# Performance work log

Hardware: AMD Instinct MI355X
Metric: run time of the kernel (lower is better)

## Reference

```python
import jax, jax.numpy as jnp
import numpy as np

N_E = 8192
E_DIM = 64
EPS = 1e-12  # torch F.normalize eps


def l2_normalize(x):
    n = jnp.linalg.norm(x, axis=-1, keepdims=True)
    return x / jnp.maximum(n, EPS)


def setup_inputs() -> dict:
    key = jax.random.key(0)
    k1, k2 = jax.random.split(key)
    z = jax.random.normal(k1, (8, E_DIM, 64, 64), dtype=jnp.float32)  # [B, C, H, W]
    # init: uniform(-1/n_e, 1/n_e) then L2-normalized (l2_norm=True)
    emb = jax.random.uniform(k2, (N_E, E_DIM), dtype=jnp.float32,
                             minval=-1.0 / N_E, maxval=1.0 / N_E)
    emb = l2_normalize(emb)
    return {"z": z, "embedding": emb}


def reference(z, embedding):
    # b c h w -> b h w c
    zt = jnp.transpose(z, (0, 2, 3, 1))
    zn = l2_normalize(zt)                      # l2_norm=True path
    z_flat = zn.reshape(-1, zn.shape[-1])      # [B*H*W, e_dim]
    e = l2_normalize(embedding)                # [n_e, e_dim]

    # squared L2 distances: ||z||^2 + ||e||^2 - 2 z e^T
    d = (jnp.sum(z_flat ** 2, axis=1, keepdims=True)
         + jnp.sum(e ** 2, axis=1)
         - 2.0 * jnp.einsum('bd,nd->bn', z_flat, e))  # [B*H*W, n_e]

    min_encoding_indices = jnp.argmin(d, axis=1)       # [B*H*W]
    z_q = e[min_encoding_indices].reshape(zn.shape)    # gather codebook

    # straight-through estimator (eval mode: commit_loss is None)
    z_q = zn + jax.lax.stop_gradient(z_q - zn)
    z_q = jnp.transpose(z_q, (0, 3, 1, 2))             # b h w c -> b c h w
    return z_q, min_encoding_indices
```

## Files before the change

### kernel.cpp

```cpp
#include <hip/hip_runtime.h>


#define NPIX 32768
#define NE   8192
#define EDIM 64
#define HW   4096
#define NSTAGE 128
#define KSPLIT 8
#define CPS  (NE / KSPLIT)
#define NSTG (CPS / NSTAGE)
#define MARGIN1 6.0e-4f
#define MARGIN2 3.0e-5f
#define NSET 2
#define RSCL 2048.0f
#define RINV 4.8828125e-4f

typedef _Float16 f16x8 __attribute__((ext_vector_type(8)));
typedef float f32x4  __attribute__((ext_vector_type(4)));

__device__ __forceinline__ short f2h_bits(float x) {
    _Float16 h = (_Float16)x;
    short s; __builtin_memcpy(&s, &h, 2); return s;
}
__device__ __forceinline__ float h_hi_f(float x) {
    return (float)(_Float16)x;
}
__device__ __forceinline__ unsigned int order_u32(float f) {
    unsigned int s = __float_as_uint(f);
    return (s & 0x80000000u) ? ~s : (s | 0x80000000u);
}
__device__ __forceinline__ void gload_lds16(const void* g, void* l) {
    __builtin_amdgcn_global_load_lds(
        (const __attribute__((address_space(1))) void*)g,
        (__attribute__((address_space(3))) void*)l, 16, 0, 0);
}

__global__ __launch_bounds__(256) void k_prep(const float* __restrict__ emb,
                                              const float* __restrict__ z,
                                              float* __restrict__ e_norm,
                                              float* __restrict__ se_half,
                                              short* __restrict__ esw,
                                              short* __restrict__ eswl,
                                              float* __restrict__ zn,
                                              unsigned* __restrict__ counter) {
    if (blockIdx.x == 0 && threadIdx.x == 0) { counter[0] = 0u; counter[1] = 0u; }
    if (blockIdx.x < NE / 4) {
        const int wave = threadIdx.x >> 6;
        const int lane = threadIdx.x & 63;
        const int n = blockIdx.x * 4 + wave;
        float v = emb[n * EDIM + lane];
        float ss = v * v;
        #pragma unroll
        for (int off = 32; off; off >>= 1) ss += __shfl_xor(ss, off, 64);
        const float inv = 1.0f / fmaxf(sqrtf(ss), 1e-12f);
        const float en = v * inv;
        e_norm[n * EDIM + lane] = en;
        const float hf = h_hi_f(en);
        const int grp = n >> 6, cs = n & 63;
        const int sub = cs >> 4, colb = cs & 15;
        const int o = lane >> 3, j = lane & 7;
        const int slot = ((o & 3) * 16 + colb) * 8 + j;
        const int off16 = grp * 4096 + (sub * 2 + (o >> 2)) * 512 + slot;
        esw[off16]  = f2h_bits(en);
        eswl[off16] = f2h_bits((en - hf) * RSCL);
        float s2 = en * en;
        #pragma unroll
        for (int off = 32; off; off >>= 1) s2 += __shfl_xor(s2, off, 64);
        if (lane == 0) se_half[n] = 0.5f * s2;
    } else {
        const int p = (blockIdx.x - NE / 4) * 256 + threadIdx.x;
        const int b = p >> 12, hw = p & (HW - 1);
        const float* zp = z + b * (EDIM * HW) + hw;
        float v[EDIM];
        #pragma unroll
        for (int c = 0; c < EDIM; ++c) v[c] = zp[c * HW];
        float ss = 0.0f;
        #pragma unroll
        for (int c = 0; c < EDIM; ++c) ss = fmaf(v[c], v[c], ss);
        const float inv = 1.0f / fmaxf(sqrtf(ss), 1e-12f);
        #pragma unroll
        for (int c4 = 0; c4 < 16; ++c4) {
            float4 o;
            o.x = v[c4 * 4 + 0] * inv;
            o.y = v[c4 * 4 + 1] * inv;
            o.z = v[c4 * 4 + 2] * inv;
            o.w = v[c4 * 4 + 3] * inv;
            *(float4*)(zn + p * EDIM + c4 * 4) = o;
        }
    }
}

__global__ __launch_bounds__(256, 1) void k_mfma(const float* __restrict__ zn,
                                                 const short* __restrict__ esw,
                                                 float2* __restrict__ pv,
                                                 unsigned* __restrict__ pi)
{
    __shared__ __align__(16) short es[2][NSTAGE * EDIM];

    const int tid  = threadIdx.x;
    const int wave = tid >> 6, lane = tid & 63;
    const int quad = lane >> 4, col = lane & 15;
    const int p0   = blockIdx.x * 128 + wave * 32;
    const int g    = blockIdx.y;
    const int kbase = g * CPS;

    f16x8 ah[NSET][2];
    #pragma unroll
    for (int s = 0; s < NSET; ++s) {
        const float* zr = zn + (p0 + s * 16 + col) * EDIM;
        #pragma unroll
        for (int kc = 0; kc < 2; ++kc) {
            float f[8];
            *(float4*)(f + 0) = *(const float4*)(zr + kc * 32 + quad * 8 + 0);
            *(float4*)(f + 4) = *(const float4*)(zr + kc * 32 + quad * 8 + 4);
            #pragma unroll
            for (int i = 0; i < 8; ++i) ah[s][kc][i] = (_Float16)f[i];
        }
    }

    float b1[NSET][4], b2[NSET][4];
    #pragma unroll
    for (int s = 0; s < NSET; ++s)
        #pragma unroll
        for (int r = 0; r < 4; ++r) { b1[s][r] = 0.0f; b2[s][r] = 0.0f; }

    const f32x4 cini = {2.0f, 2.0f, 2.0f, 2.0f};

    const int combo0 = wave * 4;
    const char* gsrc0 = (const char*)esw + (size_t)kbase * 128
                        + combo0 * 1024 + lane * 16;
    #pragma unroll
    for (int it = 0; it < 4; ++it)
        gload_lds16(gsrc0 + it * 1024, (char*)&es[0][0] + (combo0 + it) * 1024);

    for (int nb = 0; nb < NSTG; ++nb) {
        const int cur = nb & 1;
        __syncthreads();
        if (nb + 1 < NSTG) {
            const char* gsrc = gsrc0 + (size_t)(nb + 1) * (NSTAGE * EDIM * 2);
            #pragma unroll
            for (int it = 0; it < 4; ++it)
                gload_lds16(gsrc + it * 1024,
                            (char*)&es[cur ^ 1][0] + (combo0 + it) * 1024);
        }

        const short* esb = es[cur];
        #pragma unroll
        for (int sub = 0; sub < 8; ++sub) {
            const short* base = esb + sub * 1024;
            const f16x8 bh0 = *(const f16x8*)(base + lane * 8);
            const f16x8 bh1 = *(const f16x8*)(base + 512 + lane * 8);
            const unsigned sid = (unsigned)((nb << 3) | sub);
            #pragma unroll
            for (int s = 0; s < NSET; ++s) {
                f32x4 acc;
                acc = __builtin_amdgcn_mfma_f32_16x16x32_f16(ah[s][0], bh0, cini, 0, 0, 0);
                acc = __builtin_amdgcn_mfma_f32_16x16x32_f16(ah[s][1], bh1, acc, 0, 0, 0);
                #pragma unroll
                for (int r = 0; r < 4; ++r) {
                    const float v = __uint_as_float(
                        (__float_as_uint(acc[r]) & 0xFFFFFFC0u) | sid);
                    b2[s][r] = __builtin_amdgcn_fmed3f(v, b2[s][r], b1[s][r]);
                    b1[s][r] = fmaxf(b1[s][r], v);
                }
            }
        }
    }

    int i1[NSET][4];
    #pragma unroll
    for (int s = 0; s < NSET; ++s)
        #pragma unroll
        for (int r = 0; r < 4; ++r) {
            const unsigned id6 = __float_as_uint(b1[s][r]) & 63u;
            i1[s][r] = kbase + (int)(id6 << 4) + col;
        }

    #pragma unroll
    for (int m = 1; m <= 8; m <<= 1) {
        #pragma unroll
        for (int s = 0; s < NSET; ++s)
            #pragma unroll
            for (int r = 0; r < 4; ++r) {
                const float ob1 = __shfl_xor(b1[s][r], m, 64);
                const int   oi1 = __shfl_xor(i1[s][r], m, 64);
                const float ob2 = __shfl_xor(b2[s][r], m, 64);
                const bool take = (ob1 > b1[s][r]) || (ob1 == b1[s][r] && oi1 < i1[s][r]);
                b2[s][r] = fmaxf(fmaxf(b2[s][r], ob2), fminf(b1[s][r], ob1));
                b1[s][r] = take ? ob1 : b1[s][r];
                i1[s][r] = take ? oi1 : i1[s][r];
            }
    }
    if (col == 0) {
        #pragma unroll
        for (int s = 0; s < NSET; ++s)
            #pragma unroll
            for (int r = 0; r < 4; ++r) {
                const int p = p0 + s * 16 + quad * 4 + r;
                pv[g * NPIX + p] = make_float2(b1[s][r], b2[s][r]);
                pi[g * NPIX + p] = (unsigned)i1[s][r];
            }
    }
}

__global__ __launch_bounds__(256) void k_merge(const float2* __restrict__ pv,
                                               const unsigned* __restrict__ pi,
                                               unsigned* __restrict__ idx_arr,
                                               unsigned* __restrict__ list,
                                               unsigned* __restrict__ counter,
                                               unsigned long long* __restrict__ packed) {
    const int p = blockIdx.x * 256 + threadIdx.x;
    float2 v[KSPLIT]; unsigned ix[KSPLIT];
    #pragma unroll
    for (int gg = 0; gg < KSPLIT; ++gg) { v[gg] = pv[gg * NPIX + p]; ix[gg] = pi[gg * NPIX + p]; }
    float b1 = v[0].x; unsigned i1 = ix[0]; int win = 0;
    #pragma unroll
    for (int gg = 1; gg < KSPLIT; ++gg)
        if (v[gg].x > b1) { b1 = v[gg].x; i1 = ix[gg]; win = gg; }
    float b2 = -3.0e38f;
    #pragma unroll
    for (int gg = 0; gg < KSPLIT; ++gg) {
        b2 = fmaxf(b2, v[gg].y);
        if (gg != win) b2 = fmaxf(b2, v[gg].x);
    }
    const bool fl = (b1 - b2 < MARGIN1);
    idx_arr[p] = i1 | (fl ? 0x80000000u : 0u);
    if (fl) {
        packed[p] = ~0ull;
        const unsigned pos = atomicAdd(&counter[0], 1u);
        if (pos < NPIX) list[pos] = p;
    }
}

__global__ __launch_bounds__(256, 1) void k_rechk2(const float* __restrict__ zn,
                                                   const short* __restrict__ esw,
                                                   const short* __restrict__ eswl,
                                                   const unsigned* __restrict__ list,
                                                   const unsigned* __restrict__ counter,
                                                   float2* __restrict__ pv,
                                                   unsigned* __restrict__ pi)
{
    __shared__ __align__(16) short es[2][2][NSTAGE * EDIM];

    int cnt = (int)counter[0]; if (cnt > NPIX) cnt = NPIX;
    const int ib = blockIdx.x * 128;
    if (ib >= cnt) return;

    const int tid  = threadIdx.x;
    const int wave = tid >> 6, lane = tid & 63;
    const int quad = lane >> 4, col = lane & 15;
    const int g    = blockIdx.y;
    const int kbase = g * CPS;

    f16x8 ah[NSET][2], al[NSET][2];
    #pragma unroll
    for (int s = 0; s < NSET; ++s) {
        int item = ib + wave * 32 + s * 16 + col;
        if (item > cnt - 1) item = cnt - 1;
        const float* zr = zn + (size_t)list[item] * EDIM;
        #pragma unroll
        for (int kc = 0; kc < 2; ++kc) {
            float f[8];
            *(float4*)(f + 0) = *(const float4*)(zr + kc * 32 + quad * 8 + 0);
            *(float4*)(f + 4) = *(const float4*)(zr + kc * 32 + quad * 8 + 4);
            #pragma unroll
            for (int i = 0; i < 8; ++i) {
                ah[s][kc][i] = (_Float16)f[i];
                al[s][kc][i] = (_Float16)((f[i] - h_hi_f(f[i])) * RSCL);
            }
        }
    }

    float b1[NSET][4], b2[NSET][4]; int i1[NSET][4];
    #pragma unroll
    for (int s = 0; s < NSET; ++s)
        #pragma unroll
        for (int r = 0; r < 4; ++r) { b1[s][r] = 0.0f; b2[s][r] = 0.0f; i1[s][r] = 0; }

    const f32x4 cini = {2.0f, 2.0f, 2.0f, 2.0f};
    const f32x4 zero = {0.0f, 0.0f, 0.0f, 0.0f};

    const int combo0 = wave * 4;
    const char* ghi0 = (const char*)esw  + (size_t)kbase * 128 + combo0 * 1024 + lane * 16;
    const char* glo0 = (const char*)eswl + (size_t)kbase * 128 + combo0 * 1024 + lane * 16;
    #pragma unroll
    for (int it = 0; it < 4; ++it) {
        gload_lds16(ghi0 + it * 1024, (char*)&es[0][0][0] + (combo0 + it) * 1024);
        gload_lds16(glo0 + it * 1024, (char*)&es[0][1][0] + (combo0 + it) * 1024);
    }

    for (int nb = 0; nb < NSTG; ++nb) {
        const int cur = nb & 1;
        const int n0 = kbase + nb * NSTAGE;
        __syncthreads();
        if (nb + 1 < NSTG) {
            const size_t soff = (size_t)(nb + 1) * (NSTAGE * EDIM * 2);
            #pragma unroll
            for (int it = 0; it < 4; ++it) {
                gload_lds16(ghi0 + soff + it * 1024,
                            (char*)&es[cur ^ 1][0][0] + (combo0 + it) * 1024);
                gload_lds16(glo0 + soff + it * 1024,
                            (char*)&es[cur ^ 1][1][0] + (combo0 + it) * 1024);
            }
        }

        const short* eh = es[cur][0];
        const short* el = es[cur][1];
        #pragma unroll
        for (int sub = 0; sub < 8; ++sub) {
            const f16x8 bh0 = *(const f16x8*)(eh + sub * 1024 + lane * 8);
            const f16x8 bh1 = *(const f16x8*)(eh + sub * 1024 + 512 + lane * 8);
            const f16x8 bl0 = *(const f16x8*)(el + sub * 1024 + lane * 8);
            const f16x8 bl1 = *(const f16x8*)(el + sub * 1024 + 512 + lane * 8);
            const int nglob = n0 + sub * 16 + col;
            #pragma unroll
            for (int s = 0; s < NSET; ++s) {
                f32x4 acc;
                acc = __builtin_amdgcn_mfma_f32_16x16x32_f16(ah[s][0], bh0, cini, 0, 0, 0);
                acc = __builtin_amdgcn_mfma_f32_16x16x32_f16(ah[s][1], bh1, acc, 0, 0, 0);
                f32x4 cor;
                cor = __builtin_amdgcn_mfma_f32_16x16x32_f16(al[s][0], bh0, zero, 0, 0, 0);
                cor = __builtin_amdgcn_mfma_f32_16x16x32_f16(ah[s][0], bl0, cor, 0, 0, 0);
                cor = __builtin_amdgcn_mfma_f32_16x16x32_f16(al[s][1], bh1, cor, 0, 0, 0);
                cor = __builtin_amdgcn_mfma_f32_16x16x32_f16(ah[s][1], bl1, cor, 0, 0, 0);
                #pragma unroll
                for (int r = 0; r < 4; ++r) {
                    const float v = fmaf(cor[r], RINV, acc[r]);
                    b2[s][r] = __builtin_amdgcn_fmed3f(v, b2[s][r], b1[s][r]);
                    const bool t = v > b1[s][r];
                    b1[s][r] = fmaxf(b1[s][r], v);
                    i1[s][r] = t ? nglob : i1[s][r];
                }
            }
        }
    }

    #pragma unroll
    for (int m = 1; m <= 8; m <<= 1) {
        #pragma unroll
        for (int s = 0; s < NSET; ++s)
            #pragma unroll
            for (int r = 0; r < 4; ++r) {
                const float ob1 = __shfl_xor(b1[s][r], m, 64);
                const int   oi1 = __shfl_xor(i1[s][r], m, 64);
                const float ob2 = __shfl_xor(b2[s][r], m, 64);
                const bool take = (ob1 > b1[s][r]) || (ob1 == b1[s][r] && oi1 < i1[s][r]);
                b2[s][r] = fmaxf(fmaxf(b2[s][r], ob2), fminf(b1[s][r], ob1));
                b1[s][r] = take ? ob1 : b1[s][r];
                i1[s][r] = take ? oi1 : i1[s][r];
            }
    }
    if (col == 0) {
        #pragma unroll
        for (int s = 0; s < NSET; ++s)
            #pragma unroll
            for (int r = 0; r < 4; ++r) {
                const int item = ib + wave * 32 + s * 16 + quad * 4 + r;
                if (item < cnt) {
                    pv[g * NPIX + item] = make_float2(b1[s][r], b2[s][r]);
                    pi[g * NPIX + item] = (unsigned)i1[s][r];
                }
            }
    }
}

__global__ __launch_bounds__(256) void k_merge2(const float2* __restrict__ pv,
                                                const unsigned* __restrict__ pi,
                                                const unsigned* __restrict__ list,
                                                unsigned* __restrict__ counter,
                                                unsigned* __restrict__ list2,
                                                unsigned long long* __restrict__ packed) {
    const int item = blockIdx.x * 256 + threadIdx.x;
    int cnt = (int)counter[0]; if (cnt > NPIX) cnt = NPIX;
    if (item >= cnt) return;
    const unsigned p = list[item];
    float2 v[KSPLIT]; unsigned ix[KSPLIT];
    #pragma unroll
    for (int gg = 0; gg < KSPLIT; ++gg) { v[gg] = pv[gg * NPIX + item]; ix[gg] = pi[gg * NPIX + item]; }
    float b1 = v[0].x; unsigned i1 = ix[0]; int win = 0;
    #pragma unroll
    for (int gg = 1; gg < KSPLIT; ++gg)
        if (v[gg].x > b1) { b1 = v[gg].x; i1 = ix[gg]; win = gg; }
    float b2 = -3.0e38f;
    #pragma unroll
    for (int gg = 0; gg < KSPLIT; ++gg) {
        b2 = fmaxf(b2, v[gg].y);
        if (gg != win) b2 = fmaxf(b2, v[gg].x);
    }
    if (b1 - b2 < MARGIN2) {
        const unsigned pos = atomicAdd(&counter[1], 1u);
        if (pos < NPIX) list2[pos] = p;
    } else {
        packed[p] = (unsigned long long)i1;
    }
}

__global__ __launch_bounds__(256) void k_recheck(const float* __restrict__ zn,
                                                 const float* __restrict__ e_norm,
                                                 const float* __restrict__ se_half,
                                                 const unsigned* __restrict__ list2,
                                                 const unsigned* __restrict__ counter,
                                                 unsigned long long* __restrict__ packed) {
    const int lane  = threadIdx.x & 63;
    const int k     = lane >> 4;
    const int m     = lane & 15;
    const int wglob = (blockIdx.x * 256 + threadIdx.x) >> 6;
    const int nwav  = (gridDim.x * 256) >> 6;
    int cnt = (int)counter[1]; if (cnt > NPIX) cnt = NPIX;
    const int nitems = cnt * 16;
    const float4* e4 = (const float4*)e_norm;

    for (int item = wglob; item < nitems; item += nwav) {
        const int p     = (int)list2[item >> 4];
        const int chunk = item & 15;
        const float4 zv = *(const float4*)(zn + p * EDIM + m * 4);
        float best = 3.0e38f; int bidx = 0;
        for (int t4 = 0; t4 < 32; ++t4) {
            float s[4]; int n[4];
            #pragma unroll
            for (int j = 0; j < 4; ++j) {
                n[j] = chunk * 512 + (t4 * 4 + j) * 4 + k;
                const float4 ev = e4[n[j] * 16 + m];
                s[j] = fmaf(zv.w, ev.w, fmaf(zv.z, ev.z,
                       fmaf(zv.y, ev.y, zv.x * ev.x)));
            }
            #pragma unroll
            for (int j = 0; j < 4; ++j) s[j] += __shfl_xor(s[j], 1, 64);
            #pragma unroll
            for (int j = 0; j < 4; ++j) s[j] += __shfl_xor(s[j], 2, 64);
            #pragma unroll
            for (int j = 0; j < 4; ++j) s[j] += __shfl_xor(s[j], 4, 64);
            #pragma unroll
            for (int j = 0; j < 4; ++j) s[j] += __shfl_xor(s[j], 8, 64);
            #pragma unroll
            for (int j = 0; j < 4; ++j) {
                const float d = se_half[n[j]] - s[j];
                if (d < best) { best = d; bidx = n[j]; }
            }
        }
        #pragma unroll
        for (int mm = 1; mm <= 32; mm <<= 1) {
            const float ob = __shfl_xor(best, mm, 64);
            const int   oi = __shfl_xor(bidx, mm, 64);
            if (ob < best || (ob == best && oi < bidx)) { best = ob; bidx = oi; }
        }
        if (lane == 0) {
            const unsigned long long key =
                ((unsigned long long)order_u32(best) << 32) | (unsigned)bidx;
            atomicMin(&packed[p], key);
        }
    }
}

__global__ __launch_bounds__(256) void k_finalize(const unsigned* __restrict__ idx_arr,
                                                  const unsigned long long* __restrict__ packed,
                                                  const float* __restrict__ e_norm,
                                                  float* __restrict__ out) {
    const int pl = threadIdx.x & 63;
    const int q  = threadIdx.x >> 6;
    const int p  = blockIdx.x * 64 + pl;
    const unsigned v = idx_arr[p];
    const int bidx = (v & 0x80000000u) ? (int)(packed[p] & 0xFFFFFFFFull)
                                       : (int)v;
    if (q == 0) out[NPIX * EDIM + p] = (float)bidx;
    const int b = p >> 12, hw = p & (HW - 1);
    float* op = out + b * (EDIM * HW) + hw;
    const float4* ep4 = (const float4*)(e_norm + bidx * EDIM + q * 16);
    #pragma unroll
    for (int j = 0; j < 4; ++j) {
        const float4 e = ep4[j];
        const int c = q * 16 + j * 4;
        op[(c + 0) * HW] = e.x; op[(c + 1) * HW] = e.y;
        op[(c + 2) * HW] = e.z; op[(c + 3) * HW] = e.w;
    }
}

extern "C" void kernel_launch(void* const* d_in, const int* in_sizes, int n_in,
                              void* d_out, int out_size, void* d_ws, size_t ws_size,
                              hipStream_t stream) {
    const float* z   = (const float*)d_in[0];
    const float* emb = (const float*)d_in[1];
    float* out = (float*)d_out;

    float* e_norm  = (float*)d_ws;
    float* se_half = e_norm + NE * EDIM;
    short* esw  = (short*)(se_half + NE);
    short* eswl = esw + NE * EDIM;
    float* zn = (float*)(eswl + NE * EDIM);
    unsigned* idx_arr = (unsigned*)(zn + NPIX * EDIM);
    unsigned* list    = idx_arr + NPIX;
    unsigned* list2   = list + NPIX;
    unsigned* counter = list2 + NPIX;
    unsigned long long* packed = (unsigned long long*)(counter + 64);
    float2*   pv = (float2*)(packed + NPIX);
    unsigned* pi = (unsigned*)(pv + KSPLIT * NPIX);

    k_prep<<<NE / 4 + NPIX / 256, 256, 0, stream>>>(emb, z, e_norm, se_half,
                                                    esw, eswl, zn, counter);
    k_mfma<<<dim3(NPIX / 128, KSPLIT), 256, 0, stream>>>(zn, esw, pv, pi);
    k_merge<<<NPIX / 256, 256, 0, stream>>>(pv, pi, idx_arr, list, counter, packed);
    k_rechk2<<<dim3(NPIX / 128, KSPLIT), 256, 0, stream>>>(zn, esw, eswl, list,
                                                           counter, pv, pi);
    k_merge2<<<NPIX / 256, 256, 0, stream>>>(pv, pi, list, counter, list2, packed);
    k_recheck<<<512, 256, 0, stream>>>(zn, e_norm, se_half, list2, counter, packed);
    k_finalize<<<NPIX / 64, 256, 0, stream>>>(idx_arr, packed, e_norm, out);
}
```

Measured before the change: 188.3 us.

## Fuse second merge, exact recheck and finalize; split refine pass 32 ways

Removes the k_merge2, k_recheck and k_finalize kernels and the packed atomicMin buffer. A single k_final kernel now merges the refinement partials, runs the exact fp32 rescan per block for escaped pixels, and writes the outputs. The refine kernel now uses a capped list of 8192 items and splits the codebook 32 ways instead of 8, giving more blocks for a small candidate list. This cuts two launches and their global round trips. In exchange, escaped pixels are rescanned serially inside a block, and pixels beyond the 8192 cap fall back to a full exact scan.

```diff
diff --git a/kernel.cpp b/kernel.cpp
--- a/kernel.cpp
+++ b/kernel.cpp
@@ -9,6 +9,10 @@
 #define KSPLIT 8
 #define CPS  (NE / KSPLIT)
 #define NSTG (CPS / NSTAGE)
+#define KS2  32
+#define CPS2 (NE / KS2)
+#define NSTG2 (CPS2 / NSTAGE)
+#define CAP2 8192
 #define MARGIN1 6.0e-4f
 #define MARGIN2 3.0e-5f
 #define NSET 2
@@ -43,7 +47,7 @@
                                               short* __restrict__ eswl,
                                               float* __restrict__ zn,
                                               unsigned* __restrict__ counter) {
-    if (blockIdx.x == 0 && threadIdx.x == 0) { counter[0] = 0u; counter[1] = 0u; }
+    if (blockIdx.x == 0 && threadIdx.x == 0) { counter[0] = 0u; }
     if (blockIdx.x < NE / 4) {
         const int wave = threadIdx.x >> 6;
         const int lane = threadIdx.x & 63;
@@ -207,8 +211,7 @@
                                                const unsigned* __restrict__ pi,
                                                unsigned* __restrict__ idx_arr,
                                                unsigned* __restrict__ list,
-                                               unsigned* __restrict__ counter,
-                                               unsigned long long* __restrict__ packed) {
+                                               unsigned* __restrict__ counter) {
     const int p = blockIdx.x * 256 + threadIdx.x;
     float2 v[KSPLIT]; unsigned ix[KSPLIT];
     #pragma unroll
@@ -223,12 +226,12 @@
         b2 = fmaxf(b2, v[gg].y);
         if (gg != win) b2 = fmaxf(b2, v[gg].x);
     }
-    const bool fl = (b1 - b2 < MARGIN1);
-    idx_arr[p] = i1 | (fl ? 0x80000000u : 0u);
-    if (fl) {
-        packed[p] = ~0ull;
+    if (b1 - b2 < MARGIN1) {
         const unsigned pos = atomicAdd(&counter[0], 1u);
-        if (pos < NPIX) list[pos] = p;
+        if (pos < CAP2) list[pos] = p;
+        idx_arr[p] = 0x80000000u | pos;
+    } else {
+        idx_arr[p] = i1;
     }
 }
 
@@ -242,15 +245,15 @@
 {
     __shared__ __align__(16) short es[2][2][NSTAGE * EDIM];
 
-    int cnt = (int)counter[0]; if (cnt > NPIX) cnt = NPIX;
+    int cnt = (int)counter[0]; if (cnt > CAP2) cnt = CAP2;
     const int ib = blockIdx.x * 128;
     if (ib >= cnt) return;
 
     const int tid  = threadIdx.x;
     const int wave = tid >> 6, lane = tid & 63;
     const int quad = lane >> 4, col = lane & 15;
-    const int g    = blockIdx.y;
-    const int kbase = g * CPS;
+    const int g2   = blockIdx.y;
+    const int kbase = g2 * CPS2;
 
     f16x8 ah[NSET][2], al[NSET][2];
     #pragma unroll
@@ -289,11 +292,11 @@
         gload_lds16(glo0 + it * 1024, (char*)&es[0][1][0] + (combo0 + it) * 1024);
     }
 
-    for (int nb = 0; nb < NSTG; ++nb) {
+    for (int nb = 0; nb < NSTG2; ++nb) {
         const int cur = nb & 1;
         const int n0 = kbase + nb * NSTAGE;
         __syncthreads();
-        if (nb + 1 < NSTG) {
+        if (nb + 1 < NSTG2) {
             const size_t soff = (size_t)(nb + 1) * (NSTAGE * EDIM * 2);
             #pragma unroll
             for (int it = 0; it < 4; ++it) {
@@ -357,85 +360,92 @@
             for (int r = 0; r < 4; ++r) {
                 const int item = ib + wave * 32 + s * 16 + quad * 4 + r;
                 if (item < cnt) {
-                    pv[g * NPIX + item] = make_float2(b1[s][r], b2[s][r]);
-                    pi[g * NPIX + item] = (unsigned)i1[s][r];
+                    pv[g2 * CAP2 + item] = make_float2(b1[s][r], b2[s][r]);
+                    pi[g2 * CAP2 + item] = (unsigned)i1[s][r];
                 }
             }
     }
 }
 
-__global__ __launch_bounds__(256) void k_merge2(const float2* __restrict__ pv,
-                                                const unsigned* __restrict__ pi,
-                                                const unsigned* __restrict__ list,
-                                                unsigned* __restrict__ counter,
-                                                unsigned* __restrict__ list2,
-                                                unsigned long long* __restrict__ packed) {
-    const int item = blockIdx.x * 256 + threadIdx.x;
-    int cnt = (int)counter[0]; if (cnt > NPIX) cnt = NPIX;
-    if (item >= cnt) return;
-    const unsigned p = list[item];
-    float2 v[KSPLIT]; unsigned ix[KSPLIT];
-    #pragma unroll
-    for (int gg = 0; gg < KSPLIT; ++gg) { v[gg] = pv[gg * NPIX + item]; ix[gg] = pi[gg * NPIX + item]; }
-    float b1 = v[0].x; unsigned i1 = ix[0]; int win = 0;
-    #pragma unroll
-    for (int gg = 1; gg < KSPLIT; ++gg)
-        if (v[gg].x > b1) { b1 = v[gg].x; i1 = ix[gg]; win = gg; }
-    float b2 = -3.0e38f;
-    #pragma unroll
-    for (int gg = 0; gg < KSPLIT; ++gg) {
-        b2 = fmaxf(b2, v[gg].y);
-        if (gg != win) b2 = fmaxf(b2, v[gg].x);
-    }
-    if (b1 - b2 < MARGIN2) {
-        const unsigned pos = atomicAdd(&counter[1], 1u);
-        if (pos < NPIX) list2[pos] = p;
-    } else {
-        packed[p] = (unsigned long long)i1;
-    }
-}
-
-__global__ __launch_bounds__(256) void k_recheck(const float* __restrict__ zn,
-                                                 const float* __restrict__ e_norm,
-                                                 const float* __restrict__ se_half,
-                                                 const unsigned* __restrict__ list2,
-                                                 const unsigned* __restrict__ counter,
-                                                 unsigned long long* __restrict__ packed) {
-    const int lane  = threadIdx.x & 63;
-    const int k     = lane >> 4;
-    const int m     = lane & 15;
-    const int wglob = (blockIdx.x * 256 + threadIdx.x) >> 6;
-    const int nwav  = (gridDim.x * 256) >> 6;
-    int cnt = (int)counter[1]; if (cnt > NPIX) cnt = NPIX;
-    const int nitems = cnt * 16;
-    const float4* e4 = (const float4*)e_norm;
-
-    for (int item = wglob; item < nitems; item += nwav) {
-        const int p     = (int)list2[item >> 4];
-        const int chunk = item & 15;
-        const float4 zv = *(const float4*)(zn + p * EDIM + m * 4);
+__global__ __launch_bounds__(256) void k_final(const unsigned* __restrict__ idx_arr,
+                                               const float2* __restrict__ pv,
+                                               const unsigned* __restrict__ pi,
+                                               const float* __restrict__ e_norm,
+                                               const float* __restrict__ zn,
+                                               const float* __restrict__ se_half,
+                                               float* __restrict__ out) {
+    __shared__ int s_bidx[64];
+    __shared__ int s_escp[64];
+    __shared__ int s_esc;
+    __shared__ unsigned long long s_key[4];
+
+    const int tid  = threadIdx.x;
+    const int wave = tid >> 6, lane = tid & 63;
+    const int p0   = blockIdx.x * 64;
+
+    if (tid == 0) s_esc = 0;
+    __syncthreads();
+
+    if (wave == 0) {
+        const unsigned v = idx_arr[p0 + lane];
+        int bidx;
+        if (!(v & 0x80000000u)) {
+            bidx = (int)v;
+        } else {
+            const unsigned item = v & 0x7FFFFFFFu;
+            if (item >= CAP2) {
+                bidx = -1;
+            } else {
+                float b1 = -3.0e38f, b2 = -3.0e38f; unsigned i1 = 0;
+                #pragma unroll
+                for (int g2 = 0; g2 < KS2; ++g2) {
+                    const float2 vv = pv[g2 * CAP2 + item];
+                    const unsigned ii = pi[g2 * CAP2 + item];
+                    if (vv.x > b1) { b2 = fmaxf(b2, b1); b1 = vv.x; i1 = ii; }
+                    else           { b2 = fmaxf(b2, vv.x); }
+                    b2 = fmaxf(b2, vv.y);
+                }
+                bidx = (b1 - b2 < MARGIN2) ? -1 : (int)i1;
+            }
+        }
+        s_bidx[lane] = bidx;
+        if (bidx < 0) {
+            const int e = atomicAdd(&s_esc, 1);
+            s_escp[e] = lane;
+        }
+    }
+    __syncthreads();
+
+    const int nesc = s_esc;
+    for (int e = 0; e < nesc; ++e) {
+        const int p = p0 + s_escp[e];
+        const int k = lane >> 4, m = lane & 15;
+        const float4 zv = *(const float4*)(zn + (size_t)p * EDIM + m * 4);
+        const float4* e4 = (const float4*)e_norm;
         float best = 3.0e38f; int bidx = 0;
-        for (int t4 = 0; t4 < 32; ++t4) {
-            float s[4]; int n[4];
-            #pragma unroll
-            for (int j = 0; j < 4; ++j) {
-                n[j] = chunk * 512 + (t4 * 4 + j) * 4 + k;
-                const float4 ev = e4[n[j] * 16 + m];
-                s[j] = fmaf(zv.w, ev.w, fmaf(zv.z, ev.z,
-                       fmaf(zv.y, ev.y, zv.x * ev.x)));
-            }
-            #pragma unroll
-            for (int j = 0; j < 4; ++j) s[j] += __shfl_xor(s[j], 1, 64);
-            #pragma unroll
-            for (int j = 0; j < 4; ++j) s[j] += __shfl_xor(s[j], 2, 64);
-            #pragma unroll
-            for (int j = 0; j < 4; ++j) s[j] += __shfl_xor(s[j], 4, 64);
-            #pragma unroll
-            for (int j = 0; j < 4; ++j) s[j] += __shfl_xor(s[j], 8, 64);
-            #pragma unroll
-            for (int j = 0; j < 4; ++j) {
-                const float d = se_half[n[j]] - s[j];
-                if (d < best) { best = d; bidx = n[j]; }
+        for (int chunk = wave; chunk < 16; chunk += 4) {
+            for (int t4 = 0; t4 < 32; ++t4) {
+                float sdot[4]; int n[4];
+                #pragma unroll
+                for (int j = 0; j < 4; ++j) {
+                    n[j] = chunk * 512 + (t4 * 4 + j) * 4 + k;
+                    const float4 ev = e4[n[j] * 16 + m];
+                    sdot[j] = fmaf(zv.w, ev.w, fmaf(zv.z, ev.z,
+                              fmaf(zv.y, ev.y, zv.x * ev.x)));
+                }
+                #pragma unroll
+                for (int j = 0; j < 4; ++j) sdot[j] += __shfl_xor(sdot[j], 1, 64);
+                #pragma unroll
+                for (int j = 0; j < 4; ++j) sdot[j] += __shfl_xor(sdot[j], 2, 64);
+                #pragma unroll
+                for (int j = 0; j < 4; ++j) sdot[j] += __shfl_xor(sdot[j], 4, 64);
+                #pragma unroll
+                for (int j = 0; j < 4; ++j) sdot[j] += __shfl_xor(sdot[j], 8, 64);
+                #pragma unroll
+                for (int j = 0; j < 4; ++j) {
+                    const float d = se_half[n[j]] - sdot[j];
+                    if (d < best) { best = d; bidx = n[j]; }
+                }
             }
         }
         #pragma unroll
@@ -444,34 +454,31 @@
             const int   oi = __shfl_xor(bidx, mm, 64);
             if (ob < best || (ob == best && oi < bidx)) { best = ob; bidx = oi; }
         }
-        if (lane == 0) {
-            const unsigned long long key =
-                ((unsigned long long)order_u32(best) << 32) | (unsigned)bidx;
-            atomicMin(&packed[p], key);
-        }
-    }
-}
-
-__global__ __launch_bounds__(256) void k_finalize(const unsigned* __restrict__ idx_arr,
-                                                  const unsigned long long* __restrict__ packed,
-                                                  const float* __restrict__ e_norm,
-                                                  float* __restrict__ out) {
-    const int pl = threadIdx.x & 63;
-    const int q  = threadIdx.x >> 6;
-    const int p  = blockIdx.x * 64 + pl;
-    const unsigned v = idx_arr[p];
-    const int bidx = (v & 0x80000000u) ? (int)(packed[p] & 0xFFFFFFFFull)
-                                       : (int)v;
+        if (lane == 0)
+            s_key[wave] = ((unsigned long long)order_u32(best) << 32) | (unsigned)bidx;
+        __syncthreads();
+        if (tid == 0) {
+            unsigned long long kk = s_key[0];
+            #pragma unroll
+            for (int w = 1; w < 4; ++w) kk = (s_key[w] < kk) ? s_key[w] : kk;
+            s_bidx[s_escp[e]] = (int)(kk & 0xFFFFFFFFull);
+        }
+        __syncthreads();
+    }
+
+    const int p = p0 + lane;
+    const int bidx = s_bidx[lane];
+    const int q = wave;
     if (q == 0) out[NPIX * EDIM + p] = (float)bidx;
     const int b = p >> 12, hw = p & (HW - 1);
     float* op = out + b * (EDIM * HW) + hw;
-    const float4* ep4 = (const float4*)(e_norm + bidx * EDIM + q * 16);
+    const float4* ep4 = (const float4*)(e_norm + (size_t)bidx * EDIM + q * 16);
     #pragma unroll
     for (int j = 0; j < 4; ++j) {
-        const float4 e = ep4[j];
+        const float4 ev = ep4[j];
         const int c = q * 16 + j * 4;
-        op[(c + 0) * HW] = e.x; op[(c + 1) * HW] = e.y;
-        op[(c + 2) * HW] = e.z; op[(c + 3) * HW] = e.w;
+        op[(c + 0) * HW] = ev.x; op[(c + 1) * HW] = ev.y;
+        op[(c + 2) * HW] = ev.z; op[(c + 3) * HW] = ev.w;
     }
 }
 
@@ -489,19 +496,16 @@
     float* zn = (float*)(eswl + NE * EDIM);
     unsigned* idx_arr = (unsigned*)(zn + NPIX * EDIM);
     unsigned* list    = idx_arr + NPIX;
-    unsigned* list2   = list + NPIX;
-    unsigned* counter = list2 + NPIX;
-    unsigned long long* packed = (unsigned long long*)(counter + 64);
-    float2*   pv = (float2*)(packed + NPIX);
+    unsigned* counter = list + NPIX;
+    float2*   pv = (float2*)(counter + 64);
     unsigned* pi = (unsigned*)(pv + KSPLIT * NPIX);
 
     k_prep<<<NE / 4 + NPIX / 256, 256, 0, stream>>>(emb, z, e_norm, se_half,
                                                     esw, eswl, zn, counter);
     k_mfma<<<dim3(NPIX / 128, KSPLIT), 256, 0, stream>>>(zn, esw, pv, pi);
-    k_merge<<<NPIX / 256, 256, 0, stream>>>(pv, pi, idx_arr, list, counter, packed);
-    k_rechk2<<<dim3(NPIX / 128, KSPLIT), 256, 0, stream>>>(zn, esw, eswl, list,
-                                                           counter, pv, pi);
-    k_merge2<<<NPIX / 256, 256, 0, stream>>>(pv, pi, list, counter, list2, packed);
-    k_recheck<<<512, 256, 0, stream>>>(zn, e_norm, se_half, list2, counter, packed);
-    k_finalize<<<NPIX / 64, 256, 0, stream>>>(idx_arr, packed, e_norm, out);
-}
+    k_merge<<<NPIX / 256, 256, 0, stream>>>(pv, pi, idx_arr, list, counter);
+    k_rechk2<<<dim3(CAP2 / 128, KS2), 256, 0, stream>>>(zn, esw, eswl, list,
+                                                        counter, pv, pi);
+    k_final<<<NPIX / 64, 256, 0, stream>>>(idx_arr, pv, pi, e_norm, zn,
+                                           se_half, out);
+}
```

Result: slower. 299.5 us (+59.0%).

## Restructure MFMA argmin with per-wave codebook slices and capped finer-split recheck

Applied to the files above, without the earlier changes.

The main MFMA pass now gives each wave its own slice of the codebook chunk, with private LDS double buffers and explicit vmcnt waits instead of block-wide barriers. Each block handles 64 pixels, so every wave carries 4 A-fragment sets, and the per-wave top-2 results are merged through shared memory. The refinement pass is capped at 8192 flagged pixels with a 32-way codebook split to spread the small work list over more blocks. Flagged pixels beyond the cap go straight to the exact fp32 recheck, whose grid is doubled. This trades more register pressure and an extra LDS merge for fewer synchronisations and better parallelism in the recheck stage.

```diff
diff --git a/kernel.cpp b/kernel.cpp
--- a/kernel.cpp
+++ b/kernel.cpp
@@ -5,13 +5,15 @@
 #define NE   8192
 #define EDIM 64
 #define HW   4096
-#define NSTAGE 128
 #define KSPLIT 8
 #define CPS  (NE / KSPLIT)
-#define NSTG (CPS / NSTAGE)
+#define NSTAGE 128
+#define KS2  32
+#define CPS2 (NE / KS2)
+#define NSTG2 (CPS2 / NSTAGE)
+#define CAP2 8192
 #define MARGIN1 6.0e-4f
 #define MARGIN2 3.0e-5f
-#define NSET 2
 #define RSCL 2048.0f
 #define RINV 4.8828125e-4f
 
@@ -95,18 +97,21 @@
                                                  float2* __restrict__ pv,
                                                  unsigned* __restrict__ pi)
 {
-    __shared__ __align__(16) short es[2][NSTAGE * EDIM];
+    __shared__ __align__(16) short es[4][2][2048];
+    __shared__ float s_b1[4][64], s_b2[4][64];
+    __shared__ int   s_i1[4][64];
 
     const int tid  = threadIdx.x;
-    const int wave = tid >> 6, lane = tid & 63;
+    const int w    = tid >> 6, lane = tid & 63;
     const int quad = lane >> 4, col = lane & 15;
-    const int p0   = blockIdx.x * 128 + wave * 32;
+    const int p0   = blockIdx.x * 64;
     const int g    = blockIdx.y;
     const int kbase = g * CPS;
-
-    f16x8 ah[NSET][2];
-    #pragma unroll
-    for (int s = 0; s < NSET; ++s) {
+    const int cbase = kbase + w * 256;
+
+    f16x8 ah[4][2];
+    #pragma unroll
+    for (int s = 0; s < 4; ++s) {
         const float* zr = zn + (p0 + s * 16 + col) * EDIM;
         #pragma unroll
         for (int kc = 0; kc < 2; ++kc) {
@@ -118,41 +123,41 @@
         }
     }
 
-    float b1[NSET][4], b2[NSET][4];
-    #pragma unroll
-    for (int s = 0; s < NSET; ++s)
+    float b1[4][4], b2[4][4];
+    #pragma unroll
+    for (int s = 0; s < 4; ++s)
         #pragma unroll
         for (int r = 0; r < 4; ++r) { b1[s][r] = 0.0f; b2[s][r] = 0.0f; }
 
     const f32x4 cini = {2.0f, 2.0f, 2.0f, 2.0f};
 
-    const int combo0 = wave * 4;
-    const char* gsrc0 = (const char*)esw + (size_t)kbase * 128
-                        + combo0 * 1024 + lane * 16;
+    const char* gw = (const char*)esw + (size_t)cbase * 128 + lane * 16;
     #pragma unroll
     for (int it = 0; it < 4; ++it)
-        gload_lds16(gsrc0 + it * 1024, (char*)&es[0][0] + (combo0 + it) * 1024);
-
-    for (int nb = 0; nb < NSTG; ++nb) {
+        gload_lds16(gw + it * 1024, (char*)&es[w][0][0] + it * 1024);
+
+    for (int nb = 0; nb < 8; ++nb) {
         const int cur = nb & 1;
-        __syncthreads();
-        if (nb + 1 < NSTG) {
-            const char* gsrc = gsrc0 + (size_t)(nb + 1) * (NSTAGE * EDIM * 2);
+        if (nb + 1 < 8) {
+            const char* gs = gw + (size_t)(nb + 1) * 4096;
             #pragma unroll
             for (int it = 0; it < 4; ++it)
-                gload_lds16(gsrc + it * 1024,
-                            (char*)&es[cur ^ 1][0] + (combo0 + it) * 1024);
-        }
-
-        const short* esb = es[cur];
-        #pragma unroll
-        for (int sub = 0; sub < 8; ++sub) {
+                gload_lds16(gs + it * 1024, (char*)&es[w][cur ^ 1][0] + it * 1024);
+            asm volatile("s_waitcnt vmcnt(4)" ::: "memory");
+        } else {
+            asm volatile("s_waitcnt vmcnt(0)" ::: "memory");
+        }
+        __builtin_amdgcn_sched_barrier(0);
+
+        const short* esb = &es[w][cur][0];
+        #pragma unroll
+        for (int sub = 0; sub < 2; ++sub) {
             const short* base = esb + sub * 1024;
             const f16x8 bh0 = *(const f16x8*)(base + lane * 8);
             const f16x8 bh1 = *(const f16x8*)(base + 512 + lane * 8);
-            const unsigned sid = (unsigned)((nb << 3) | sub);
-            #pragma unroll
-            for (int s = 0; s < NSET; ++s) {
+            const unsigned sid = (unsigned)((w << 4) | (nb << 1) | sub);
+            #pragma unroll
+            for (int s = 0; s < 4; ++s) {
                 f32x4 acc;
                 acc = __builtin_amdgcn_mfma_f32_16x16x32_f16(ah[s][0], bh0, cini, 0, 0, 0);
                 acc = __builtin_amdgcn_mfma_f32_16x16x32_f16(ah[s][1], bh1, acc, 0, 0, 0);
@@ -167,9 +172,9 @@
         }
     }
 
-    int i1[NSET][4];
-    #pragma unroll
-    for (int s = 0; s < NSET; ++s)
+    int i1[4][4];
+    #pragma unroll
+    for (int s = 0; s < 4; ++s)
         #pragma unroll
         for (int r = 0; r < 4; ++r) {
             const unsigned id6 = __float_as_uint(b1[s][r]) & 63u;
@@ -179,7 +184,7 @@
     #pragma unroll
     for (int m = 1; m <= 8; m <<= 1) {
         #pragma unroll
-        for (int s = 0; s < NSET; ++s)
+        for (int s = 0; s < 4; ++s)
             #pragma unroll
             for (int r = 0; r < 4; ++r) {
                 const float ob1 = __shfl_xor(b1[s][r], m, 64);
@@ -193,13 +198,30 @@
     }
     if (col == 0) {
         #pragma unroll
-        for (int s = 0; s < NSET; ++s)
+        for (int s = 0; s < 4; ++s)
             #pragma unroll
             for (int r = 0; r < 4; ++r) {
-                const int p = p0 + s * 16 + quad * 4 + r;
-                pv[g * NPIX + p] = make_float2(b1[s][r], b2[s][r]);
-                pi[g * NPIX + p] = (unsigned)i1[s][r];
-            }
+                const int px = s * 16 + quad * 4 + r;
+                s_b1[w][px] = b1[s][r];
+                s_b2[w][px] = b2[s][r];
+                s_i1[w][px] = i1[s][r];
+            }
+    }
+    __syncthreads();
+    if (w == 0) {
+        float B1 = s_b1[0][lane], B2 = s_b2[0][lane];
+        int   I1 = s_i1[0][lane];
+        #pragma unroll
+        for (int ww = 1; ww < 4; ++ww) {
+            const float ob1 = s_b1[ww][lane], ob2 = s_b2[ww][lane];
+            const int   oi1 = s_i1[ww][lane];
+            const bool take = ob1 > B1;
+            B2 = fmaxf(fmaxf(B2, ob2), fminf(B1, ob1));
+            B1 = take ? ob1 : B1;
+            I1 = take ? oi1 : I1;
+        }
+        pv[g * NPIX + p0 + lane] = make_float2(B1, B2);
+        pi[g * NPIX + p0 + lane] = (unsigned)I1;
     }
 }
 
@@ -207,6 +229,7 @@
                                                const unsigned* __restrict__ pi,
                                                unsigned* __restrict__ idx_arr,
                                                unsigned* __restrict__ list,
+                                               unsigned* __restrict__ list2,
                                                unsigned* __restrict__ counter,
                                                unsigned long long* __restrict__ packed) {
     const int p = blockIdx.x * 256 + threadIdx.x;
@@ -223,12 +246,18 @@
         b2 = fmaxf(b2, v[gg].y);
         if (gg != win) b2 = fmaxf(b2, v[gg].x);
     }
-    const bool fl = (b1 - b2 < MARGIN1);
-    idx_arr[p] = i1 | (fl ? 0x80000000u : 0u);
-    if (fl) {
+    if (b1 - b2 < MARGIN1) {
         packed[p] = ~0ull;
+        idx_arr[p] = i1 | 0x80000000u;
         const unsigned pos = atomicAdd(&counter[0], 1u);
-        if (pos < NPIX) list[pos] = p;
+        if (pos < CAP2) {
+            list[pos] = p;
+        } else {
+            const unsigned q = atomicAdd(&counter[1], 1u);
+            if (q < NPIX) list2[q] = p;
+        }
+    } else {
+        idx_arr[p] = i1;
     }
 }
 
@@ -242,19 +271,19 @@
 {
     __shared__ __align__(16) short es[2][2][NSTAGE * EDIM];
 
-    int cnt = (int)counter[0]; if (cnt > NPIX) cnt = NPIX;
+    int cnt = (int)counter[0]; if (cnt > CAP2) cnt = CAP2;
     const int ib = blockIdx.x * 128;
     if (ib >= cnt) return;
 
     const int tid  = threadIdx.x;
     const int wave = tid >> 6, lane = tid & 63;
     const int quad = lane >> 4, col = lane & 15;
-    const int g    = blockIdx.y;
-    const int kbase = g * CPS;
-
-    f16x8 ah[NSET][2], al[NSET][2];
-    #pragma unroll
-    for (int s = 0; s < NSET; ++s) {
+    const int g2   = blockIdx.y;
+    const int kbase = g2 * CPS2;
+
+    f16x8 ah[2][2], al[2][2];
+    #pragma unroll
+    for (int s = 0; s < 2; ++s) {
         int item = ib + wave * 32 + s * 16 + col;
         if (item > cnt - 1) item = cnt - 1;
         const float* zr = zn + (size_t)list[item] * EDIM;
@@ -271,9 +300,9 @@
         }
     }
 
-    float b1[NSET][4], b2[NSET][4]; int i1[NSET][4];
-    #pragma unroll
-    for (int s = 0; s < NSET; ++s)
+    float b1[2][4], b2[2][4]; int i1[2][4];
+    #pragma unroll
+    for (int s = 0; s < 2; ++s)
         #pragma unroll
         for (int r = 0; r < 4; ++r) { b1[s][r] = 0.0f; b2[s][r] = 0.0f; i1[s][r] = 0; }
 
@@ -289,11 +318,11 @@
         gload_lds16(glo0 + it * 1024, (char*)&es[0][1][0] + (combo0 + it) * 1024);
     }
 
-    for (int nb = 0; nb < NSTG; ++nb) {
+    for (int nb = 0; nb < NSTG2; ++nb) {
         const int cur = nb & 1;
         const int n0 = kbase + nb * NSTAGE;
         __syncthreads();
-        if (nb + 1 < NSTG) {
+        if (nb + 1 < NSTG2) {
             const size_t soff = (size_t)(nb + 1) * (NSTAGE * EDIM * 2);
             #pragma unroll
             for (int it = 0; it < 4; ++it) {
@@ -314,7 +343,7 @@
             const f16x8 bl1 = *(const f16x8*)(el + sub * 1024 + 512 + lane * 8);
             const int nglob = n0 + sub * 16 + col;
             #pragma unroll
-            for (int s = 0; s < NSET; ++s) {
+            for (int s = 0; s < 2; ++s) {
                 f32x4 acc;
                 acc = __builtin_amdgcn_mfma_f32_16x16x32_f16(ah[s][0], bh0, cini, 0, 0, 0);
                 acc = __builtin_amdgcn_mfma_f32_16x16x32_f16(ah[s][1], bh1, acc, 0, 0, 0);
@@ -338,7 +367,7 @@
     #pragma unroll
     for (int m = 1; m <= 8; m <<= 1) {
         #pragma unroll
-        for (int s = 0; s < NSET; ++s)
+        for (int s = 0; s < 2; ++s)
             #pragma unroll
             for (int r = 0; r < 4; ++r) {
                 const float ob1 = __shfl_xor(b1[s][r], m, 64);
@@ -352,13 +381,13 @@
     }
     if (col == 0) {
         #pragma unroll
-        for (int s = 0; s < NSET; ++s)
+        for (int s = 0; s < 2; ++s)
             #pragma unroll
             for (int r = 0; r < 4; ++r) {
                 const int item = ib + wave * 32 + s * 16 + quad * 4 + r;
                 if (item < cnt) {
-                    pv[g * NPIX + item] = make_float2(b1[s][r], b2[s][r]);
-                    pi[g * NPIX + item] = (unsigned)i1[s][r];
+                    pv[g2 * CAP2 + item] = make_float2(b1[s][r], b2[s][r]);
+                    pi[g2 * CAP2 + item] = (unsigned)i1[s][r];
                 }
             }
     }
@@ -371,25 +400,21 @@
                                                 unsigned* __restrict__ list2,
                                                 unsigned long long* __restrict__ packed) {
     const int item = blockIdx.x * 256 + threadIdx.x;
-    int cnt = (int)counter[0]; if (cnt > NPIX) cnt = NPIX;
+    int cnt = (int)counter[0]; if (cnt > CAP2) cnt = CAP2;
     if (item >= cnt) return;
     const unsigned p = list[item];
-    float2 v[KSPLIT]; unsigned ix[KSPLIT];
-    #pragma unroll
-    for (int gg = 0; gg < KSPLIT; ++gg) { v[gg] = pv[gg * NPIX + item]; ix[gg] = pi[gg * NPIX + item]; }
-    float b1 = v[0].x; unsigned i1 = ix[0]; int win = 0;
-    #pragma unroll
-    for (int gg = 1; gg < KSPLIT; ++gg)
-        if (v[gg].x > b1) { b1 = v[gg].x; i1 = ix[gg]; win = gg; }
-    float b2 = -3.0e38f;
-    #pragma unroll
-    for (int gg = 0; gg < KSPLIT; ++gg) {
-        b2 = fmaxf(b2, v[gg].y);
-        if (gg != win) b2 = fmaxf(b2, v[gg].x);
+    float b1 = -3.0e38f, b2 = -3.0e38f; unsigned i1 = 0;
+    #pragma unroll
+    for (int g2 = 0; g2 < KS2; ++g2) {
+        const float2 vv = pv[g2 * CAP2 + item];
+        const unsigned ii = pi[g2 * CAP2 + item];
+        if (vv.x > b1) { b2 = fmaxf(b2, b1); b1 = vv.x; i1 = ii; }
+        else           { b2 = fmaxf(b2, vv.x); }
+        b2 = fmaxf(b2, vv.y);
     }
     if (b1 - b2 < MARGIN2) {
-        const unsigned pos = atomicAdd(&counter[1], 1u);
-        if (pos < NPIX) list2[pos] = p;
+        const unsigned q = atomicAdd(&counter[1], 1u);
+        if (q < NPIX) list2[q] = p;
     } else {
         packed[p] = (unsigned long long)i1;
     }
@@ -413,7 +438,7 @@
     for (int item = wglob; item < nitems; item += nwav) {
         const int p     = (int)list2[item >> 4];
         const int chunk = item & 15;
-        const float4 zv = *(const float4*)(zn + p * EDIM + m * 4);
+        const float4 zv = *(const float4*)(zn + (size_t)p * EDIM + m * 4);
         float best = 3.0e38f; int bidx = 0;
         for (int t4 = 0; t4 < 32; ++t4) {
             float s[4]; int n[4];
@@ -465,7 +490,7 @@
     if (q == 0) out[NPIX * EDIM + p] = (float)bidx;
     const int b = p >> 12, hw = p & (HW - 1);
     float* op = out + b * (EDIM * HW) + hw;
-    const float4* ep4 = (const float4*)(e_norm + bidx * EDIM + q * 16);
+    const float4* ep4 = (const float4*)(e_norm + (size_t)bidx * EDIM + q * 16);
     #pragma unroll
     for (int j = 0; j < 4; ++j) {
         const float4 e = ep4[j];
@@ -497,11 +522,12 @@
 
     k_prep<<<NE / 4 + NPIX / 256, 256, 0, stream>>>(emb, z, e_norm, se_half,
                                                     esw, eswl, zn, counter);
-    k_mfma<<<dim3(NPIX / 128, KSPLIT), 256, 0, stream>>>(zn, esw, pv, pi);
-    k_merge<<<NPIX / 256, 256, 0, stream>>>(pv, pi, idx_arr, list, counter, packed);
-    k_rechk2<<<dim3(NPIX / 128, KSPLIT), 256, 0, stream>>>(zn, esw, eswl, list,
-                                                           counter, pv, pi);
-    k_merge2<<<NPIX / 256, 256, 0, stream>>>(pv, pi, list, counter, list2, packed);
-    k_recheck<<<512, 256, 0, stream>>>(zn, e_norm, se_half, list2, counter, packed);
+    k_mfma<<<dim3(NPIX / 64, KSPLIT), 256, 0, stream>>>(zn, esw, pv, pi);
+    k_merge<<<NPIX / 256, 256, 0, stream>>>(pv, pi, idx_arr, list, list2,
+                                            counter, packed);
+    k_rechk2<<<dim3(CAP2 / 128, KS2), 256, 0, stream>>>(zn, esw, eswl, list,
+                                                        counter, pv, pi);
+    k_merge2<<<CAP2 / 256, 256, 0, stream>>>(pv, pi, list, counter, list2, packed);
+    k_recheck<<<1024, 256, 0, stream>>>(zn, e_norm, se_half, list2, counter, packed);
     k_finalize<<<NPIX / 64, 256, 0, stream>>>(idx_arr, packed, e_norm, out);
 }
```

Result: slower. 248.9 us (+32.2%).

## Cap second-pass recheck list, split codebook 16 ways, overflow to exact pass

Applied to the files above, without the earlier changes.

The second-pass fp16 hi/lo MFMA recheck now splits the codebook into 16 chunks with smaller 64-code LDS stages, instead of 8 chunks with 128-code stages. This doubles parallelism for the flagged pixel list. The recheck list is capped at 16384 entries: overflow pixels go straight to the exact fp32 recheck list, and the grid sizes are reduced to match the cap. The merge step reduces 16 partials with a streaming top-2 update. The final fp32 recheck gets more blocks, and some index math is widened to size_t. The aim is to cut wasted blocks and raise occupancy for the recheck, at the cost of more partial-result traffic and a slower exact path for any overflow.

```diff
diff --git a/kernel.cpp b/kernel.cpp
--- a/kernel.cpp
+++ b/kernel.cpp
@@ -9,6 +9,11 @@
 #define KSPLIT 8
 #define CPS  (NE / KSPLIT)
 #define NSTG (CPS / NSTAGE)
+#define KS2  16
+#define CPS2 (NE / KS2)
+#define NST2 64
+#define NSTG2 (CPS2 / NST2)
+#define CAP2 16384
 #define MARGIN1 6.0e-4f
 #define MARGIN2 3.0e-5f
 #define NSET 2
@@ -207,6 +212,7 @@
                                                const unsigned* __restrict__ pi,
                                                unsigned* __restrict__ idx_arr,
                                                unsigned* __restrict__ list,
+                                               unsigned* __restrict__ list2,
                                                unsigned* __restrict__ counter,
                                                unsigned long long* __restrict__ packed) {
     const int p = blockIdx.x * 256 + threadIdx.x;
@@ -223,12 +229,18 @@
         b2 = fmaxf(b2, v[gg].y);
         if (gg != win) b2 = fmaxf(b2, v[gg].x);
     }
-    const bool fl = (b1 - b2 < MARGIN1);
-    idx_arr[p] = i1 | (fl ? 0x80000000u : 0u);
-    if (fl) {
+    if (b1 - b2 < MARGIN1) {
         packed[p] = ~0ull;
+        idx_arr[p] = i1 | 0x80000000u;
         const unsigned pos = atomicAdd(&counter[0], 1u);
-        if (pos < NPIX) list[pos] = p;
+        if (pos < CAP2) {
+            list[pos] = p;
+        } else {
+            const unsigned q = atomicAdd(&counter[1], 1u);
+            if (q < NPIX) list2[q] = p;
+        }
+    } else {
+        idx_arr[p] = i1;
     }
 }
 
@@ -240,17 +252,17 @@
                                                    float2* __restrict__ pv,
                                                    unsigned* __restrict__ pi)
 {
-    __shared__ __align__(16) short es[2][2][NSTAGE * EDIM];
-
-    int cnt = (int)counter[0]; if (cnt > NPIX) cnt = NPIX;
+    __shared__ __align__(16) short es[2][2][NST2 * EDIM];
+
+    int cnt = (int)counter[0]; if (cnt > CAP2) cnt = CAP2;
     const int ib = blockIdx.x * 128;
     if (ib >= cnt) return;
 
     const int tid  = threadIdx.x;
     const int wave = tid >> 6, lane = tid & 63;
     const int quad = lane >> 4, col = lane & 15;
-    const int g    = blockIdx.y;
-    const int kbase = g * CPS;
+    const int g2   = blockIdx.y;
+    const int kbase = g2 * CPS2;
 
     f16x8 ah[NSET][2], al[NSET][2];
     #pragma unroll
@@ -280,23 +292,23 @@
     const f32x4 cini = {2.0f, 2.0f, 2.0f, 2.0f};
     const f32x4 zero = {0.0f, 0.0f, 0.0f, 0.0f};
 
-    const int combo0 = wave * 4;
+    const int combo0 = wave * 2;
     const char* ghi0 = (const char*)esw  + (size_t)kbase * 128 + combo0 * 1024 + lane * 16;
     const char* glo0 = (const char*)eswl + (size_t)kbase * 128 + combo0 * 1024 + lane * 16;
     #pragma unroll
-    for (int it = 0; it < 4; ++it) {
+    for (int it = 0; it < 2; ++it) {
         gload_lds16(ghi0 + it * 1024, (char*)&es[0][0][0] + (combo0 + it) * 1024);
         gload_lds16(glo0 + it * 1024, (char*)&es[0][1][0] + (combo0 + it) * 1024);
     }
 
-    for (int nb = 0; nb < NSTG; ++nb) {
+    for (int nb = 0; nb < NSTG2; ++nb) {
         const int cur = nb & 1;
-        const int n0 = kbase + nb * NSTAGE;
+        const int n0 = kbase + nb * NST2;
         __syncthreads();
-        if (nb + 1 < NSTG) {
-            const size_t soff = (size_t)(nb + 1) * (NSTAGE * EDIM * 2);
-            #pragma unroll
-            for (int it = 0; it < 4; ++it) {
+        if (nb + 1 < NSTG2) {
+            const size_t soff = (size_t)(nb + 1) * (NST2 * EDIM * 2);
+            #pragma unroll
+            for (int it = 0; it < 2; ++it) {
                 gload_lds16(ghi0 + soff + it * 1024,
                             (char*)&es[cur ^ 1][0][0] + (combo0 + it) * 1024);
                 gload_lds16(glo0 + soff + it * 1024,
@@ -307,7 +319,7 @@
         const short* eh = es[cur][0];
         const short* el = es[cur][1];
         #pragma unroll
-        for (int sub = 0; sub < 8; ++sub) {
+        for (int sub = 0; sub < 4; ++sub) {
             const f16x8 bh0 = *(const f16x8*)(eh + sub * 1024 + lane * 8);
             const f16x8 bh1 = *(const f16x8*)(eh + sub * 1024 + 512 + lane * 8);
             const f16x8 bl0 = *(const f16x8*)(el + sub * 1024 + lane * 8);
@@ -357,8 +369,8 @@
             for (int r = 0; r < 4; ++r) {
                 const int item = ib + wave * 32 + s * 16 + quad * 4 + r;
                 if (item < cnt) {
-                    pv[g * NPIX + item] = make_float2(b1[s][r], b2[s][r]);
-                    pi[g * NPIX + item] = (unsigned)i1[s][r];
+                    pv[g2 * CAP2 + item] = make_float2(b1[s][r], b2[s][r]);
+                    pi[g2 * CAP2 + item] = (unsigned)i1[s][r];
                 }
             }
     }
@@ -371,25 +383,21 @@
                                                 unsigned* __restrict__ list2,
                                                 unsigned long long* __restrict__ packed) {
     const int item = blockIdx.x * 256 + threadIdx.x;
-    int cnt = (int)counter[0]; if (cnt > NPIX) cnt = NPIX;
+    int cnt = (int)counter[0]; if (cnt > CAP2) cnt = CAP2;
     if (item >= cnt) return;
     const unsigned p = list[item];
-    float2 v[KSPLIT]; unsigned ix[KSPLIT];
-    #pragma unroll
-    for (int gg = 0; gg < KSPLIT; ++gg) { v[gg] = pv[gg * NPIX + item]; ix[gg] = pi[gg * NPIX + item]; }
-    float b1 = v[0].x; unsigned i1 = ix[0]; int win = 0;
-    #pragma unroll
-    for (int gg = 1; gg < KSPLIT; ++gg)
-        if (v[gg].x > b1) { b1 = v[gg].x; i1 = ix[gg]; win = gg; }
-    float b2 = -3.0e38f;
-    #pragma unroll
-    for (int gg = 0; gg < KSPLIT; ++gg) {
-        b2 = fmaxf(b2, v[gg].y);
-        if (gg != win) b2 = fmaxf(b2, v[gg].x);
+    float b1 = -3.0e38f, b2 = -3.0e38f; unsigned i1 = 0;
+    #pragma unroll
+    for (int g2 = 0; g2 < KS2; ++g2) {
+        const float2 vv = pv[g2 * CAP2 + item];
+        const unsigned ii = pi[g2 * CAP2 + item];
+        if (vv.x > b1) { b2 = fmaxf(b2, b1); b1 = vv.x; i1 = ii; }
+        else           { b2 = fmaxf(b2, vv.x); }
+        b2 = fmaxf(b2, vv.y);
     }
     if (b1 - b2 < MARGIN2) {
-        const unsigned pos = atomicAdd(&counter[1], 1u);
-        if (pos < NPIX) list2[pos] = p;
+        const unsigned q = atomicAdd(&counter[1], 1u);
+        if (q < NPIX) list2[q] = p;
     } else {
         packed[p] = (unsigned long long)i1;
     }
@@ -413,7 +421,7 @@
     for (int item = wglob; item < nitems; item += nwav) {
         const int p     = (int)list2[item >> 4];
         const int chunk = item & 15;
-        const float4 zv = *(const float4*)(zn + p * EDIM + m * 4);
+        const float4 zv = *(const float4*)(zn + (size_t)p * EDIM + m * 4);
         float best = 3.0e38f; int bidx = 0;
         for (int t4 = 0; t4 < 32; ++t4) {
             float s[4]; int n[4];
@@ -465,7 +473,7 @@
     if (q == 0) out[NPIX * EDIM + p] = (float)bidx;
     const int b = p >> 12, hw = p & (HW - 1);
     float* op = out + b * (EDIM * HW) + hw;
-    const float4* ep4 = (const float4*)(e_norm + bidx * EDIM + q * 16);
+    const float4* ep4 = (const float4*)(e_norm + (size_t)bidx * EDIM + q * 16);
     #pragma unroll
     for (int j = 0; j < 4; ++j) {
         const float4 e = ep4[j];
@@ -498,10 +506,11 @@
     k_prep<<<NE / 4 + NPIX / 256, 256, 0, stream>>>(emb, z, e_norm, se_half,
                                                     esw, eswl, zn, counter);
     k_mfma<<<dim3(NPIX / 128, KSPLIT), 256, 0, stream>>>(zn, esw, pv, pi);
-    k_merge<<<NPIX / 256, 256, 0, stream>>>(pv, pi, idx_arr, list, counter, packed);
-    k_rechk2<<<dim3(NPIX / 128, KSPLIT), 256, 0, stream>>>(zn, esw, eswl, list,
-                                                           counter, pv, pi);
-    k_merge2<<<NPIX / 256, 256, 0, stream>>>(pv, pi, list, counter, list2, packed);
-    k_recheck<<<512, 256, 0, stream>>>(zn, e_norm, se_half, list2, counter, packed);
+    k_merge<<<NPIX / 256, 256, 0, stream>>>(pv, pi, idx_arr, list, list2,
+                                            counter, packed);
+    k_rechk2<<<dim3(CAP2 / 128, KS2), 256, 0, stream>>>(zn, esw, eswl, list,
+                                                        counter, pv, pi);
+    k_merge2<<<CAP2 / 256, 256, 0, stream>>>(pv, pi, list, counter, list2, packed);
+    k_recheck<<<1024, 256, 0, stream>>>(zn, e_norm, se_half, list2, counter, packed);
     k_finalize<<<NPIX / 64, 256, 0, stream>>>(idx_arr, packed, e_norm, out);
 }
```

After: 189.3 us. No clear change (+0.5%).
